# Performance work log

Hardware: AMD Instinct MI355X
Metric: run time of the kernel (lower is better)

## Reference

```python
import jax, jax.numpy as jnp
import numpy as np

B, N, D = 8, 2048, 512   # batch, ctx_size, input_size
P, H = 16, 32            # num_pers, hidden_size


def setup_inputs() -> dict:
    key = jax.random.key(0)
    k1, k2 = jax.random.split(key)
    context = jax.random.normal(k1, (B, N, D), dtype=jnp.float32)
    # stacked weights of the 16 bias-free nn.Linear(input_size, hidden_size) layers
    # xavier-uniform-style scale: sqrt(6/(fan_in+fan_out))
    limit = np.sqrt(6.0 / (D + H)).astype(np.float32)
    W = jax.random.uniform(k2, (P, H, D), dtype=jnp.float32, minval=-limit, maxval=limit)
    ctx_mask = jnp.ones((B, N), dtype=jnp.int32)
    return {"context": context, "W": W, "ctx_mask": ctx_mask}


def reference(context, W, ctx_mask):
    # per-persona projection + relu: [P, B, N, H]
    fc = jax.nn.relu(jnp.einsum('bnd,phd->pbnh', context, W))
    # sum over personas of fc @ fc^T, then average: [B, N, N]
    att = jnp.einsum('pbnh,pbmh->bnm', fc, fc) / P
    # NOTE: original uses F.softmax(attention, dim=1) -> softmax over rows (axis=1)
    att = jax.nn.softmax(att, axis=1)
    # masked_fill with markoff_value=0 on masked columns then masked rows
    m = ctx_mask.astype(att.dtype)          # [B, N]
    att = att * m[:, None, :] * m[:, :, None]
    return att
```

## Files before the change

kernel.cpp:

```cpp
#include <hip/hip_runtime.h>

#define Bc 8
#define Nc 2048
#define Dc 512
#define PH 512
#define NN 4194304
#define NT 136

#define BM 128
#define BN 128
#define BK 32

typedef __attribute__((ext_vector_type(8))) short bf16x8;
typedef __attribute__((ext_vector_type(4))) float f32x4;

static __device__ __forceinline__ unsigned short f2b(float x) {
    union { float f; unsigned u; } v; v.f = x;
    unsigned r = v.u + 0x7fffu + ((v.u >> 16) & 1u);
    return (unsigned short)(r >> 16);
}

static __device__ __forceinline__ float b2f(unsigned short x) {
    return __builtin_bit_cast(float, (unsigned)x << 16);
}

static __device__ __forceinline__ void load16_lds(const unsigned short* g, unsigned short* l) {
    __builtin_amdgcn_global_load_lds(
        (const __attribute__((address_space(1))) void*)g,
        (__attribute__((address_space(3))) void*)l,
        16, 0, 0);
}

__global__ __launch_bounds__(256) void prep_kernel(
    const float* __restrict__ ctx, const float* __restrict__ W,
    unsigned short* __restrict__ Xb, unsigned short* __restrict__ Wb,
    float* __restrict__ rsum) {
    int t = blockIdx.x * 256 + threadIdx.x;
    if (t < 2097152) {
        float4 v = ((const float4*)ctx)[t];
        ushort4 o;
        o.x = f2b(v.x); o.y = f2b(v.y); o.z = f2b(v.z); o.w = f2b(v.w);
        ((ushort4*)Xb)[t] = o;
    }
    if (t < 65536) {
        float4 v = ((const float4*)W)[t];
        ushort4 o;
        o.x = f2b(v.x); o.y = f2b(v.y); o.z = f2b(v.z); o.w = f2b(v.w);
        ((ushort4*)Wb)[t] = o;
    }
    if (t < 4096) {
        float4 z; z.x = 0.f; z.y = 0.f; z.z = 0.f; z.w = 0.f;
        ((float4*)rsum)[t] = z;
    }
}

__global__ __launch_bounds__(256) void gemm1_relu(
    const unsigned short* __restrict__ Xb, const unsigned short* __restrict__ Wb,
    unsigned short* __restrict__ F) {
    __shared__ unsigned short As[BM * BK];
    __shared__ unsigned short Bs[BN * BK];
    const int tid = threadIdx.x;
    const int lane = tid & 63;
    const int wave = tid >> 6;
    const int wm = wave >> 1, wn = wave & 1;
    const int bid = blockIdx.x;
    const int row0 = ((bid & 7) + ((bid >> 5) << 3)) * BM;
    const int col0 = ((bid >> 3) & 3) * BN;

    f32x4 acc[4][4] = {};

    for (int k0 = 0; k0 < Dc; k0 += BK) {
#pragma unroll
        for (int j = 0; j < 2; ++j) {
            int e = j * 256 + tid;
            int rr = e >> 2, cc = e & 3;
            load16_lds(&Xb[(size_t)(row0 + rr) * Dc + k0 + cc * 8], &As[e * 8]);
            load16_lds(&Wb[(size_t)(col0 + rr) * Dc + k0 + cc * 8], &Bs[e * 8]);
        }
        __syncthreads();

        bf16x8 af[4], bfr[4];
#pragma unroll
        for (int i = 0; i < 4; ++i) {
            af[i]  = *(const bf16x8*)&As[(wm * 64 + i * 16 + (lane & 15)) * BK + (lane >> 4) * 8];
            bfr[i] = *(const bf16x8*)&Bs[(wn * 64 + i * 16 + (lane & 15)) * BK + (lane >> 4) * 8];
        }
#pragma unroll
        for (int mi = 0; mi < 4; ++mi)
#pragma unroll
            for (int ni = 0; ni < 4; ++ni)
                acc[mi][ni] = __builtin_amdgcn_mfma_f32_16x16x32_bf16(af[mi], bfr[ni], acc[mi][ni], 0, 0, 0);
        __syncthreads();
    }

#pragma unroll
    for (int mi = 0; mi < 4; ++mi) {
#pragma unroll
        for (int ni = 0; ni < 4; ++ni) {
            int col  = col0 + wn * 64 + ni * 16 + (lane & 15);
            int rowb = row0 + wm * 64 + mi * 16 + ((lane >> 4) << 2);
#pragma unroll
            for (int r = 0; r < 4; ++r) {
                float v = fmaxf(acc[mi][ni][r], 0.0f);
                F[(size_t)(rowb + r) * PH + col] = f2b(v);
            }
        }
    }
}

__global__ __launch_bounds__(256) void gemm2_store(
    const unsigned short* __restrict__ F, float* __restrict__ rsum,
    unsigned short* __restrict__ Ework) {
    __shared__ unsigned short As[BM * BK];
    __shared__ unsigned short Bs[BN * BK];
    const int tid = threadIdx.x;
    const int lane = tid & 63;
    const int wave = tid >> 6;
    const int wm = wave >> 1, wn = wave & 1;
    const int l15 = lane & 15, q = lane >> 4;
    const int b = blockIdx.x & 7;
    const int idx = blockIdx.x >> 3;

    int j = 0;
    while (((j + 1) * (j + 2) / 2) <= idx) ++j;
    int i = idx - j * (j + 1) / 2;
    const int row0 = i * BM;
    const int col0 = j * BN;
    const unsigned short* Fb = F + (size_t)b * Nc * PH;

    f32x4 acc[4][4] = {};

    for (int k0 = 0; k0 < PH; k0 += BK) {
#pragma unroll
        for (int jj = 0; jj < 2; ++jj) {
            int e = jj * 256 + tid;
            int rr = e >> 2, cc = e & 3;
            load16_lds(&Fb[(size_t)(row0 + rr) * PH + k0 + cc * 8], &As[e * 8]);
            load16_lds(&Fb[(size_t)(col0 + rr) * PH + k0 + cc * 8], &Bs[e * 8]);
        }
        __syncthreads();

        bf16x8 af[4], bfr[4];
#pragma unroll
        for (int qq = 0; qq < 4; ++qq) {
            af[qq]  = *(const bf16x8*)&As[(wm * 64 + qq * 16 + l15) * BK + q * 8];
            bfr[qq] = *(const bf16x8*)&Bs[(wn * 64 + qq * 16 + l15) * BK + q * 8];
        }
#pragma unroll
        for (int mi = 0; mi < 4; ++mi)
#pragma unroll
            for (int ni = 0; ni < 4; ++ni)
                acc[mi][ni] = __builtin_amdgcn_mfma_f32_16x16x32_bf16(af[mi], bfr[ni], acc[mi][ni], 0, 0, 0);
        __syncthreads();
    }

    unsigned short* Et = Ework + (size_t)(b * NT + idx) * 16384;

    float csum[4] = {0.f, 0.f, 0.f, 0.f};
    float rsm[4][4];
#pragma unroll
    for (int mi = 0; mi < 4; ++mi)
#pragma unroll
        for (int r = 0; r < 4; ++r) rsm[mi][r] = 0.f;

#pragma unroll
    for (int mi = 0; mi < 4; ++mi) {
#pragma unroll
        for (int ni = 0; ni < 4; ++ni) {
#pragma unroll
            for (int r = 0; r < 4; ++r) {
                float e = __expf(acc[mi][ni][r] * 0.0625f - 32.0f);
                Et[(wm * 64 + mi * 16 + (q << 2) + r) * 128 + wn * 64 + ni * 16 + l15] = f2b(e);
                csum[ni] += e;
                rsm[mi][r] += e;
            }
        }
    }
#pragma unroll
    for (int ni = 0; ni < 4; ++ni) {
        float s = csum[ni];
        s += __shfl_xor(s, 16);
        s += __shfl_xor(s, 32);
        if ((lane >> 4) == 0)
            atomicAdd(&rsum[b * Nc + col0 + wn * 64 + ni * 16 + lane], s);
    }
    if (i != j) {
#pragma unroll
        for (int mi = 0; mi < 4; ++mi) {
#pragma unroll
            for (int r = 0; r < 4; ++r) {
                float s = rsm[mi][r];
                s += __shfl_xor(s, 1);
                s += __shfl_xor(s, 2);
                s += __shfl_xor(s, 4);
                s += __shfl_xor(s, 8);
                if ((lane & 15) == 0)
                    atomicAdd(&rsum[b * Nc + row0 + wm * 64 + mi * 16 + ((lane >> 4) << 2) + r], s);
            }
        }
    }
}

__global__ __launch_bounds__(256) void scatter_out(
    const unsigned short* __restrict__ Ework, const float* __restrict__ rsum,
    const int* __restrict__ mask, float* __restrict__ out) {
    __shared__ float Ts[32 * 132];
    __shared__ float invA[128];
    __shared__ float invB[128];
    const int tid = threadIdx.x;
    const int b = blockIdx.x & 7;
    const int idx = blockIdx.x >> 3;

    int j = 0;
    while (((j + 1) * (j + 2) / 2) <= idx) ++j;
    int i = idx - j * (j + 1) / 2;
    const int row0 = i * BM;
    const int col0 = j * BN;

    const unsigned short* Et = Ework + (size_t)(b * NT + idx) * 16384;
    const float* rsb  = rsum + b * Nc;
    const int*   mb   = mask + b * Nc;
    float* outb = out + (size_t)b * NN;

    if (tid < 128)       invA[tid]       = (float)mb[col0 + tid]       / rsb[col0 + tid];
    else                 invB[tid - 128] = (float)mb[row0 + tid - 128] / rsb[row0 + tid - 128];
    __syncthreads();

    const int cl = tid >> 3, f0 = tid & 7;
    const int mc = tid >> 1, h  = tid & 1;

    for (int ci = 0; ci < 4; ++ci) {
        if (ci) __syncthreads();
        const int r = ci * 32 + cl;
        const int n = row0 + r;
        const float mrow = (float)mb[n];
#pragma unroll
        for (int g = 0; g < 2; ++g) {
            const int c0 = 64 * g + 8 * f0;
            union { int4 iv; unsigned short hv[8]; } u;
            u.iv = *(const int4*)&Et[r * 128 + c0];
            float ev[8];
#pragma unroll
            for (int k = 0; k < 8; ++k) ev[k] = b2f(u.hv[k]);
            *(float4*)&Ts[cl * 132 + c0]     = *(float4*)&ev[0];
            *(float4*)&Ts[cl * 132 + c0 + 4] = *(float4*)&ev[4];
            float4 iv0 = *(const float4*)&invA[c0];
            float4 iv1 = *(const float4*)&invA[c0 + 4];
            float4 o0, o1;
            o0.x = ev[0] * iv0.x * mrow;
            o0.y = ev[1] * iv0.y * mrow;
            o0.z = ev[2] * iv0.z * mrow;
            o0.w = ev[3] * iv0.w * mrow;
            o1.x = ev[4] * iv1.x * mrow;
            o1.y = ev[5] * iv1.y * mrow;
            o1.z = ev[6] * iv1.z * mrow;
            o1.w = ev[7] * iv1.w * mrow;
            *(float4*)&outb[(size_t)n * Nc + col0 + c0]     = o0;
            *(float4*)&outb[(size_t)n * Nc + col0 + c0 + 4] = o1;
        }
        if (i == j) continue;
        __syncthreads();
        const int a = col0 + mc;
        const float mcol = (float)mb[a];
        const int lb0 = ci * 32 + 16 * h;
        const int nb0 = row0 + lb0;
#pragma unroll
        for (int u = 0; u < 4; ++u) {
            float4 iv = *(const float4*)&invB[lb0 + 4 * u];
            float4 o;
            o.x = Ts[(16 * h + 4 * u + 0) * 132 + mc] * iv.x * mcol;
            o.y = Ts[(16 * h + 4 * u + 1) * 132 + mc] * iv.y * mcol;
            o.z = Ts[(16 * h + 4 * u + 2) * 132 + mc] * iv.z * mcol;
            o.w = Ts[(16 * h + 4 * u + 3) * 132 + mc] * iv.w * mcol;
            *(float4*)&outb[(size_t)a * Nc + nb0 + 4 * u] = o;
        }
    }
}

__global__ __launch_bounds__(256) void invr_kernel(
    const float* __restrict__ rsum, const int* __restrict__ mask,
    float* __restrict__ invr) {
    int t = blockIdx.x * 256 + threadIdx.x;
    if (t < Bc * Nc) invr[t] = (float)mask[t] / rsum[t];
}

__global__ __launch_bounds__(256) void gemm1_relu_fb(
    const unsigned short* __restrict__ Xb, const unsigned short* __restrict__ Wb,
    unsigned short* __restrict__ F) {
    __shared__ unsigned short As[BM * BK];
    __shared__ unsigned short Bs[BN * BK];
    const int tid = threadIdx.x;
    const int lane = tid & 63;
    const int wave = tid >> 6;
    const int wm = wave >> 1, wn = wave & 1;
    const int row0 = blockIdx.y * BM;
    const int col0 = blockIdx.x * BN;

    f32x4 acc[4][4] = {};

    for (int k0 = 0; k0 < Dc; k0 += BK) {
#pragma unroll
        for (int j = 0; j < 2; ++j) {
            int e = j * 256 + tid;
            int rr = e >> 2, cc = e & 3;
            load16_lds(&Xb[(size_t)(row0 + rr) * Dc + k0 + cc * 8], &As[e * 8]);
            load16_lds(&Wb[(size_t)(col0 + rr) * Dc + k0 + cc * 8], &Bs[e * 8]);
        }
        __syncthreads();

        bf16x8 af[4], bfr[4];
#pragma unroll
        for (int i = 0; i < 4; ++i) {
            af[i]  = *(const bf16x8*)&As[(wm * 64 + i * 16 + (lane & 15)) * BK + (lane >> 4) * 8];
            bfr[i] = *(const bf16x8*)&Bs[(wn * 64 + i * 16 + (lane & 15)) * BK + (lane >> 4) * 8];
        }
#pragma unroll
        for (int mi = 0; mi < 4; ++mi)
#pragma unroll
            for (int ni = 0; ni < 4; ++ni)
                acc[mi][ni] = __builtin_amdgcn_mfma_f32_16x16x32_bf16(af[mi], bfr[ni], acc[mi][ni], 0, 0, 0);
        __syncthreads();
    }

#pragma unroll
    for (int mi = 0; mi < 4; ++mi) {
#pragma unroll
        for (int ni = 0; ni < 4; ++ni) {
            int col  = col0 + wn * 64 + ni * 16 + (lane & 15);
            int rowb = row0 + wm * 64 + mi * 16 + ((lane >> 4) << 2);
#pragma unroll
            for (int r = 0; r < 4; ++r) {
                float v = fmaxf(acc[mi][ni][r], 0.0f);
                F[(size_t)(rowb + r) * PH + col] = f2b(v);
            }
        }
    }
}

__global__ __launch_bounds__(256) void gemm2_rsum(
    const unsigned short* __restrict__ F, float* __restrict__ rsum) {
    __shared__ unsigned short As[BM * BK];
    __shared__ unsigned short Bs[BN * BK];
    const int tid = threadIdx.x;
    const int lane = tid & 63;
    const int wave = tid >> 6;
    const int wm = wave >> 1, wn = wave & 1;
    const int b = blockIdx.y;

    int idx = blockIdx.x;
    int j = 0;
    while (((j + 1) * (j + 2) / 2) <= idx) ++j;
    int i = idx - j * (j + 1) / 2;
    const int row0 = i * BM;
    const int col0 = j * BN;
    const unsigned short* Fb = F + (size_t)b * Nc * PH;

    f32x4 acc[4][4] = {};

    for (int k0 = 0; k0 < PH; k0 += BK) {
#pragma unroll
        for (int jj = 0; jj < 2; ++jj) {
            int e = jj * 256 + tid;
            int rr = e >> 2, cc = e & 3;
            load16_lds(&Fb[(size_t)(row0 + rr) * PH + k0 + cc * 8], &As[e * 8]);
            load16_lds(&Fb[(size_t)(col0 + rr) * PH + k0 + cc * 8], &Bs[e * 8]);
        }
        __syncthreads();

        bf16x8 af[4], bfr[4];
#pragma unroll
        for (int q = 0; q < 4; ++q) {
            af[q]  = *(const bf16x8*)&As[(wm * 64 + q * 16 + (lane & 15)) * BK + (lane >> 4) * 8];
            bfr[q] = *(const bf16x8*)&Bs[(wn * 64 + q * 16 + (lane & 15)) * BK + (lane >> 4) * 8];
        }
#pragma unroll
        for (int mi = 0; mi < 4; ++mi)
#pragma unroll
            for (int ni = 0; ni < 4; ++ni)
                acc[mi][ni] = __builtin_amdgcn_mfma_f32_16x16x32_bf16(af[mi], bfr[ni], acc[mi][ni], 0, 0, 0);
        __syncthreads();
    }

    float csum[4] = {0.f, 0.f, 0.f, 0.f};
    float rsm[4][4];
#pragma unroll
    for (int mi = 0; mi < 4; ++mi)
#pragma unroll
        for (int r = 0; r < 4; ++r) rsm[mi][r] = 0.f;

#pragma unroll
    for (int mi = 0; mi < 4; ++mi) {
#pragma unroll
        for (int ni = 0; ni < 4; ++ni) {
#pragma unroll
            for (int r = 0; r < 4; ++r) {
                float e = __expf(acc[mi][ni][r] * 0.0625f - 32.0f);
                csum[ni] += e;
                rsm[mi][r] += e;
            }
        }
    }
#pragma unroll
    for (int ni = 0; ni < 4; ++ni) {
        float s = csum[ni];
        s += __shfl_xor(s, 16);
        s += __shfl_xor(s, 32);
        if ((lane >> 4) == 0)
            atomicAdd(&rsum[b * Nc + col0 + wn * 64 + ni * 16 + lane], s);
    }
    if (i != j) {
#pragma unroll
        for (int mi = 0; mi < 4; ++mi) {
#pragma unroll
            for (int r = 0; r < 4; ++r) {
                float s = rsm[mi][r];
                s += __shfl_xor(s, 1);
                s += __shfl_xor(s, 2);
                s += __shfl_xor(s, 4);
                s += __shfl_xor(s, 8);
                if ((lane & 15) == 0)
                    atomicAdd(&rsum[b * Nc + row0 + wm * 64 + mi * 16 + ((lane >> 4) << 2) + r], s);
            }
        }
    }
}

__global__ __launch_bounds__(256) void gemm2_write_sym(
    const unsigned short* __restrict__ F, const float* __restrict__ invr,
    const int* __restrict__ mask, float* __restrict__ out) {
    __shared__ unsigned short As[BM * BK];
    __shared__ unsigned short Bs[BN * BK];
    __shared__ float Ts[32 * 132];
    const int tid = threadIdx.x;
    const int lane = tid & 63;
    const int wave = tid >> 6;
    const int wm = wave >> 1, wn = wave & 1;
    const int l15 = lane & 15, q = lane >> 4;
    const int b = blockIdx.y;

    int idx = blockIdx.x;
    int j = 0;
    while (((j + 1) * (j + 2) / 2) <= idx) ++j;
    int i = idx - j * (j + 1) / 2;
    const int row0 = i * BM;
    const int col0 = j * BN;
    const unsigned short* Fb = F + (size_t)b * Nc * PH;

    f32x4 acc[4][4] = {};

    for (int k0 = 0; k0 < PH; k0 += BK) {
#pragma unroll
        for (int jj = 0; jj < 2; ++jj) {
            int e = jj * 256 + tid;
            int rr = e >> 2, cc = e & 3;
            load16_lds(&Fb[(size_t)(row0 + rr) * PH + k0 + cc * 8], &As[e * 8]);
            load16_lds(&Fb[(size_t)(col0 + rr) * PH + k0 + cc * 8], &Bs[e * 8]);
        }
        __syncthreads();

        bf16x8 af[4], bfr[4];
#pragma unroll
        for (int qq = 0; qq < 4; ++qq) {
            af[qq]  = *(const bf16x8*)&As[(wm * 64 + qq * 16 + l15) * BK + q * 8];
            bfr[qq] = *(const bf16x8*)&Bs[(wn * 64 + qq * 16 + l15) * BK + q * 8];
        }
#pragma unroll
        for (int mi = 0; mi < 4; ++mi)
#pragma unroll
            for (int ni = 0; ni < 4; ++ni)
                acc[mi][ni] = __builtin_amdgcn_mfma_f32_16x16x32_bf16(af[mi], bfr[ni], acc[mi][ni], 0, 0, 0);
        __syncthreads();
    }

#pragma unroll
    for (int mi = 0; mi < 4; ++mi)
#pragma unroll
        for (int ni = 0; ni < 4; ++ni)
#pragma unroll
            for (int r = 0; r < 4; ++r)
                acc[mi][ni][r] = __expf(acc[mi][ni][r] * 0.0625f - 32.0f);

    float* outb = out + (size_t)b * NN;

    float iv[4];
#pragma unroll
    for (int ni = 0; ni < 4; ++ni)
        iv[ni] = invr[b * Nc + col0 + wn * 64 + ni * 16 + l15];
#pragma unroll
    for (int mi = 0; mi < 4; ++mi) {
        int rowb = row0 + wm * 64 + mi * 16 + (q << 2);
        const int4 mr4 = *(const int4*)&mask[b * Nc + rowb];
        float mr[4] = {(float)mr4.x, (float)mr4.y, (float)mr4.z, (float)mr4.w};
#pragma unroll
        for (int ni = 0; ni < 4; ++ni) {
            int col = col0 + wn * 64 + ni * 16 + l15;
#pragma unroll
            for (int r = 0; r < 4; ++r)
                outb[(size_t)(rowb + r) * Nc + col] = acc[mi][ni][r] * iv[ni] * mr[r];
        }
    }

    if (i != j) {
#pragma unroll
        for (int ci = 0; ci < 4; ++ci) {
            __syncthreads();
            if (wn == (ci >> 1)) {
#pragma unroll
                for (int ni2 = 0; ni2 < 2; ++ni2) {
                    int ni = (ci & 1) * 2 + ni2;
#pragma unroll
                    for (int mi = 0; mi < 4; ++mi) {
                        *(float4*)&Ts[(ni2 * 16 + l15) * 132 + wm * 64 + mi * 16 + (q << 2)] =
                            *(float4*)&acc[mi][ni];
                    }
                }
            }
            __syncthreads();
            int cl = tid >> 3;
            int f0 = tid & 7;
            int nn = col0 + ci * 32 + cl;
            float mrow = (float)mask[b * Nc + nn];
            float* orow = &outb[(size_t)nn * Nc + row0];
#pragma unroll
            for (int g = 0; g < 4; ++g) {
                int f = f0 + g * 8;
                float4 ev  = *(float4*)&Ts[cl * 132 + 4 * f];
                float4 iv4 = *(const float4*)&invr[b * Nc + row0 + 4 * f];
                float4 o;
                o.x = ev.x * iv4.x * mrow;
                o.y = ev.y * iv4.y * mrow;
                o.z = ev.z * iv4.z * mrow;
                o.w = ev.w * iv4.w * mrow;
                *(float4*)&orow[4 * f] = o;
            }
        }
    }
}

extern "C" void kernel_launch(void* const* d_in, const int* in_sizes, int n_in,
                              void* d_out, int out_size, void* d_ws, size_t ws_size,
                              hipStream_t stream) {
    const float* ctx  = (const float*)d_in[0];
    const float* W    = (const float*)d_in[1];
    const int*   mask = (const int*)d_in[2];
    float* out = (float*)d_out;

    char* ws = (char*)d_ws;

    const size_t NEED = 52494336;

    if (ws_size >= NEED) {
        unsigned short* Ework = (unsigned short*)ws;
        unsigned short* Xb    = (unsigned short*)ws;
        unsigned short* Wb    = (unsigned short*)(ws + 16777216);
        unsigned short* F     = (unsigned short*)(ws + 35651584);
        float*          rsum  = (float*)(ws + 52428800);

        prep_kernel<<<8192, 256, 0, stream>>>(ctx, W, Xb, Wb, rsum);
        gemm1_relu<<<512, 256, 0, stream>>>(Xb, Wb, F);
        gemm2_store<<<1088, 256, 0, stream>>>(F, rsum, Ework);
        scatter_out<<<1088, 256, 0, stream>>>(Ework, rsum, mask, out);
    } else {
        unsigned short* Xb = (unsigned short*)ws;
        unsigned short* Wb = (unsigned short*)(ws + 16777216);
        unsigned short* F  = (unsigned short*)(ws + 16777216 + 524288);
        float* rsum        = (float*)(ws + 16777216 + 524288 + 16777216);
        float* invr        = (float*)(ws + 16777216 + 524288 + 16777216 + 65536);

        prep_kernel<<<8192, 256, 0, stream>>>(ctx, W, Xb, Wb, rsum);
        gemm1_relu_fb<<<dim3(4, 128), 256, 0, stream>>>(Xb, Wb, F);
        gemm2_rsum<<<dim3(136, 8), 256, 0, stream>>>(F, rsum);
        invr_kernel<<<64, 256, 0, stream>>>(rsum, mask, invr);
        gemm2_write_sym<<<dim3(136, 8), 256, 0, stream>>>(F, invr, mask, out);
    }
}
```

Baseline: 229.9 us.

## Fuse fp32-to-bf16 conversion into gemm1 and share tile on diagonal gemm2 blocks

Removes the separate prep kernel by having gemm1 load fp32 context and weights directly, convert them to bf16 with a packed conversion instruction and store them into LDS. rsum is now zeroed with a memset instead. In gemm2, diagonal tiles skip the duplicate B-tile load and read both operands from the A tile. The trade-off is that gemm1 loses the async global-to-LDS path and reads twice the bytes per tile through registers. It also saves the intermediate bf16 buffer round-trip and one launch.

```diff
diff --git a/kernel.cpp b/kernel.cpp
--- a/kernel.cpp
+++ b/kernel.cpp
@@ -24,6 +24,12 @@
     return __builtin_bit_cast(float, (unsigned)x << 16);
 }
 
+static __device__ __forceinline__ unsigned pk2(float lo, float hi) {
+    unsigned r;
+    asm("v_cvt_pk_bf16_f32 %0, %1, %2" : "=v"(r) : "v"(lo), "v"(hi));
+    return r;
+}
+
 static __device__ __forceinline__ void load16_lds(const unsigned short* g, unsigned short* l) {
     __builtin_amdgcn_global_load_lds(
         (const __attribute__((address_space(1))) void*)g,
@@ -31,31 +37,8 @@
         16, 0, 0);
 }
 
-__global__ __launch_bounds__(256) void prep_kernel(
+__global__ __launch_bounds__(256) void gemm1_fused(
     const float* __restrict__ ctx, const float* __restrict__ W,
-    unsigned short* __restrict__ Xb, unsigned short* __restrict__ Wb,
-    float* __restrict__ rsum) {
-    int t = blockIdx.x * 256 + threadIdx.x;
-    if (t < 2097152) {
-        float4 v = ((const float4*)ctx)[t];
-        ushort4 o;
-        o.x = f2b(v.x); o.y = f2b(v.y); o.z = f2b(v.z); o.w = f2b(v.w);
-        ((ushort4*)Xb)[t] = o;
-    }
-    if (t < 65536) {
-        float4 v = ((const float4*)W)[t];
-        ushort4 o;
-        o.x = f2b(v.x); o.y = f2b(v.y); o.z = f2b(v.z); o.w = f2b(v.w);
-        ((ushort4*)Wb)[t] = o;
-    }
-    if (t < 4096) {
-        float4 z; z.x = 0.f; z.y = 0.f; z.z = 0.f; z.w = 0.f;
-        ((float4*)rsum)[t] = z;
-    }
-}
-
-__global__ __launch_bounds__(256) void gemm1_relu(
-    const unsigned short* __restrict__ Xb, const unsigned short* __restrict__ Wb,
     unsigned short* __restrict__ F) {
     __shared__ unsigned short As[BM * BK];
     __shared__ unsigned short Bs[BN * BK];
@@ -70,12 +53,25 @@
     f32x4 acc[4][4] = {};
 
     for (int k0 = 0; k0 < Dc; k0 += BK) {
+        int4 aw[2], bw[2];
 #pragma unroll
         for (int j = 0; j < 2; ++j) {
             int e = j * 256 + tid;
             int rr = e >> 2, cc = e & 3;
-            load16_lds(&Xb[(size_t)(row0 + rr) * Dc + k0 + cc * 8], &As[e * 8]);
-            load16_lds(&Wb[(size_t)(col0 + rr) * Dc + k0 + cc * 8], &Bs[e * 8]);
+            const float4* ga = (const float4*)&ctx[(size_t)(row0 + rr) * Dc + k0 + cc * 8];
+            const float4* gb = (const float4*)&W[(size_t)(col0 + rr) * Dc + k0 + cc * 8];
+            float4 a0 = ga[0], a1 = ga[1];
+            float4 b0 = gb[0], b1 = gb[1];
+            aw[j].x = pk2(a0.x, a0.y); aw[j].y = pk2(a0.z, a0.w);
+            aw[j].z = pk2(a1.x, a1.y); aw[j].w = pk2(a1.z, a1.w);
+            bw[j].x = pk2(b0.x, b0.y); bw[j].y = pk2(b0.z, b0.w);
+            bw[j].z = pk2(b1.x, b1.y); bw[j].w = pk2(b1.z, b1.w);
+        }
+#pragma unroll
+        for (int j = 0; j < 2; ++j) {
+            int e = j * 256 + tid;
+            *(int4*)&As[e * 8] = aw[j];
+            *(int4*)&Bs[e * 8] = bw[j];
         }
         __syncthreads();
 
@@ -126,6 +122,7 @@
     int i = idx - j * (j + 1) / 2;
     const int row0 = i * BM;
     const int col0 = j * BN;
+    const bool offd = (i != j);
     const unsigned short* Fb = F + (size_t)b * Nc * PH;
 
     f32x4 acc[4][4] = {};
@@ -136,15 +133,23 @@
             int e = jj * 256 + tid;
             int rr = e >> 2, cc = e & 3;
             load16_lds(&Fb[(size_t)(row0 + rr) * PH + k0 + cc * 8], &As[e * 8]);
-            load16_lds(&Fb[(size_t)(col0 + rr) * PH + k0 + cc * 8], &Bs[e * 8]);
+            if (offd)
+                load16_lds(&Fb[(size_t)(col0 + rr) * PH + k0 + cc * 8], &Bs[e * 8]);
         }
         __syncthreads();
 
         bf16x8 af[4], bfr[4];
 #pragma unroll
-        for (int qq = 0; qq < 4; ++qq) {
-            af[qq]  = *(const bf16x8*)&As[(wm * 64 + qq * 16 + l15) * BK + q * 8];
-            bfr[qq] = *(const bf16x8*)&Bs[(wn * 64 + qq * 16 + l15) * BK + q * 8];
+        for (int qq = 0; qq < 4; ++qq)
+            af[qq] = *(const bf16x8*)&As[(wm * 64 + qq * 16 + l15) * BK + q * 8];
+        if (offd) {
+#pragma unroll
+            for (int qq = 0; qq < 4; ++qq)
+                bfr[qq] = *(const bf16x8*)&Bs[(wn * 64 + qq * 16 + l15) * BK + q * 8];
+        } else {
+#pragma unroll
+            for (int qq = 0; qq < 4; ++qq)
+                bfr[qq] = *(const bf16x8*)&As[(wn * 64 + qq * 16 + l15) * BK + q * 8];
         }
 #pragma unroll
         for (int mi = 0; mi < 4; ++mi)
@@ -184,7 +189,7 @@
         if ((lane >> 4) == 0)
             atomicAdd(&rsum[b * Nc + col0 + wn * 64 + ni * 16 + lane], s);
     }
-    if (i != j) {
+    if (offd) {
 #pragma unroll
         for (int mi = 0; mi < 4; ++mi) {
 #pragma unroll
@@ -277,6 +282,29 @@
     }
 }
 
+__global__ __launch_bounds__(256) void prep_kernel(
+    const float* __restrict__ ctx, const float* __restrict__ W,
+    unsigned short* __restrict__ Xb, unsigned short* __restrict__ Wb,
+    float* __restrict__ rsum) {
+    int t = blockIdx.x * 256 + threadIdx.x;
+    if (t < 2097152) {
+        float4 v = ((const float4*)ctx)[t];
+        ushort4 o;
+        o.x = f2b(v.x); o.y = f2b(v.y); o.z = f2b(v.z); o.w = f2b(v.w);
+        ((ushort4*)Xb)[t] = o;
+    }
+    if (t < 65536) {
+        float4 v = ((const float4*)W)[t];
+        ushort4 o;
+        o.x = f2b(v.x); o.y = f2b(v.y); o.z = f2b(v.z); o.w = f2b(v.w);
+        ((ushort4*)Wb)[t] = o;
+    }
+    if (t < 4096) {
+        float4 z; z.x = 0.f; z.y = 0.f; z.z = 0.f; z.w = 0.f;
+        ((float4*)rsum)[t] = z;
+    }
+}
+
 __global__ __launch_bounds__(256) void invr_kernel(
     const float* __restrict__ rsum, const int* __restrict__ mask,
     float* __restrict__ invr) {
@@ -551,13 +579,11 @@
 
     if (ws_size >= NEED) {
         unsigned short* Ework = (unsigned short*)ws;
-        unsigned short* Xb    = (unsigned short*)ws;
-        unsigned short* Wb    = (unsigned short*)(ws + 16777216);
         unsigned short* F     = (unsigned short*)(ws + 35651584);
         float*          rsum  = (float*)(ws + 52428800);
 
-        prep_kernel<<<8192, 256, 0, stream>>>(ctx, W, Xb, Wb, rsum);
-        gemm1_relu<<<512, 256, 0, stream>>>(Xb, Wb, F);
+        hipMemsetAsync(rsum, 0, Bc * Nc * sizeof(float), stream);
+        gemm1_fused<<<512, 256, 0, stream>>>(ctx, W, F);
         gemm2_store<<<1088, 256, 0, stream>>>(F, rsum, Ework);
         scatter_out<<<1088, 256, 0, stream>>>(Ework, rsum, mask, out);
     } else {
```

Result: no change. 230.4 us (+0.2%).
